# Optimization experiments

Measured on AMD Instinct MI355X. Metric: run time of the kernel, lower is better.

The kernel has to match this reference:

```python
import jax, jax.numpy as jnp
import numpy as np

DIM, NHEADS = 1024, 16
HD = DIM // NHEADS
ROPE_BASE = 10000.0


def rope_cos_sin(seq_len, hd):
    inv_freq = 1.0 / (ROPE_BASE ** (jnp.arange(0, hd, 2, dtype=jnp.float32) / hd))
    t = jnp.arange(seq_len, dtype=jnp.float32)
    freqs = jnp.outer(t, inv_freq)              # [N, hd/2]
    emb = jnp.concatenate([freqs, freqs], -1)   # [N, hd]
    return jnp.cos(emb), jnp.sin(emb)


def rotate_half(x):
    h = x.shape[-1] // 2
    return jnp.concatenate([-x[..., h:], x[..., :h]], -1)


def setup_inputs() -> dict:
    key = jax.random.key(0)
    ks = jax.random.split(key, 5)
    B, N = 1, 2048
    x = jax.random.normal(ks[0], (B, N, DIM), jnp.float32)
    wq = jax.random.normal(ks[1], (DIM, DIM), jnp.float32) * 0.02
    wk = jax.random.normal(ks[2], (DIM, DIM), jnp.float32) * 0.02
    wv = jax.random.normal(ks[3], (DIM, DIM), jnp.float32) * 0.02
    wp = jax.random.normal(ks[4], (DIM, DIM), jnp.float32) * 0.02
    return {"x": x, "wq": wq, "wk": wk, "wv": wv, "wp": wp}


def reference(x, wq, wk, wv, wp):
    B, N, D = x.shape
    H, hd = NHEADS, HD
    # nn.Linear: y = x @ W.T (weights stored [out, in])
    q = (x @ wq.T).reshape(B, N, H, hd)
    k = (x @ wk.T).reshape(B, N, H, hd)
    v = (x @ wv.T).reshape(B, N, H, hd)
    cos, sin = rope_cos_sin(N, hd)
    cos = cos[None, :, None, :]
    sin = sin[None, :, None, :]
    q = q * cos + rotate_half(q) * sin
    k = k * cos + rotate_half(k) * sin
    # SDPA (no mask, non-causal, eval -> no dropout)
    scale = 1.0 / jnp.sqrt(jnp.float32(hd))
    logits = jnp.einsum("bqhd,bkhd->bhqk", q, k) * scale
    attn = jax.nn.softmax(logits, axis=-1)
    out = jnp.einsum("bhqk,bkhd->bqhd", attn, v).reshape(B, N, D)
    return out @ wp.T
```

## Files before the change

### kernel.cpp

```cpp
#include <hip/hip_runtime.h>

typedef short s16x8 __attribute__((ext_vector_type(8)));
typedef float f32x4 __attribute__((ext_vector_type(4)));

__device__ __forceinline__ unsigned short f2bf(float f) {
    unsigned int u = __float_as_uint(f);
    u += 0x7fff + ((u >> 16) & 1);
    return (unsigned short)(u >> 16);
}
__device__ __forceinline__ float bf2f(unsigned short h) {
    return __uint_as_float(((unsigned int)h) << 16);
}
__device__ __forceinline__ f32x4 mfma16(s16x8 a, s16x8 b, f32x4 c) {
    return __builtin_amdgcn_mfma_f32_16x16x32_bf16(a, b, c, 0, 0, 0);
}
__device__ __forceinline__ void async16(const void* g, void* l) {
    __builtin_amdgcn_global_load_lds(
        (const __attribute__((address_space(1))) void*)g,
        (__attribute__((address_space(3))) void*)l, 16, 0, 0);
}

__global__ __launch_bounds__(256) void convert_all(
    const float* __restrict__ x,  const float* __restrict__ wq,
    const float* __restrict__ wk, const float* __restrict__ wv,
    const float* __restrict__ wp,
    unsigned short* __restrict__ xb, unsigned short* __restrict__ wqkvb,
    unsigned short* __restrict__ wpb)
{
    const size_t XN = 2048u * 1024u, WN = 1024u * 1024u;
    size_t e = ((size_t)blockIdx.x * 256 + threadIdx.x) * 4;
    const float* s; unsigned short* d;
    if (e < XN)                { s = x  + e;               d = xb    + e; }
    else if (e < XN + WN)      { s = wq + (e - XN);        d = wqkvb + (e - XN); }
    else if (e < XN + 2 * WN)  { s = wk + (e - XN - WN);   d = wqkvb + (e - XN); }
    else if (e < XN + 3 * WN)  { s = wv + (e - XN - 2*WN); d = wqkvb + (e - XN); }
    else                       { s = wp + (e - XN - 3*WN); d = wpb   + (e - XN - 3*WN); }
    float4 v = *(const float4*)s;
    ushort4 o;
    o.x = f2bf(v.x); o.y = f2bf(v.y); o.z = f2bf(v.z); o.w = f2bf(v.w);
    *(ushort4*)d = o;
}

template<int BM, int BN, int C32>
__global__ __launch_bounds__(256) void gemm_mfma(
    const unsigned short* __restrict__ A,
    const unsigned short* __restrict__ B,
    void* __restrict__ C, int Ntot)
{
    constexpr int MT = BM / 32, NT = BN / 32;
    __shared__ unsigned short As[BM * 64];
    __shared__ unsigned short Bs[BN * 64];

    const int tid  = threadIdx.x;
    const int wave = tid >> 6, lane = tid & 63;
    const int l16  = lane & 15, quad = lane >> 4;
    const int m0   = blockIdx.y * BM, n0 = blockIdx.x * BN;
    const int wm   = (wave & 1) * (BM / 2), wn = (wave >> 1) * (BN / 2);

    const int srow = lane >> 3;
    const int scol = (lane & 7) * 8;

    f32x4 acc[MT][NT] = {};

    for (int k0 = 0; k0 < 1024; k0 += 64) {
        #pragma unroll
        for (int i = 0; i < MT; i++) {
            int j = wave * MT + i;
            async16(A + (size_t)(m0 + j * 8 + srow) * 1024 + k0 + scol, &As[j * 512]);
        }
        #pragma unroll
        for (int i = 0; i < NT; i++) {
            int j = wave * NT + i;
            async16(B + (size_t)(n0 + j * 8 + srow) * 1024 + k0 + scol, &Bs[j * 512]);
        }
        __syncthreads();

        #pragma unroll
        for (int ks = 0; ks < 2; ks++) {
            s16x8 af[MT], bfr[NT];
            #pragma unroll
            for (int mt = 0; mt < MT; mt++)
                af[mt] = *(const s16x8*)&As[(wm + mt * 16 + l16) * 64 + ks * 32 + quad * 8];
            #pragma unroll
            for (int nt = 0; nt < NT; nt++)
                bfr[nt] = *(const s16x8*)&Bs[(wn + nt * 16 + l16) * 64 + ks * 32 + quad * 8];
            #pragma unroll
            for (int mt = 0; mt < MT; mt++)
                #pragma unroll
                for (int nt = 0; nt < NT; nt++)
                    acc[mt][nt] = mfma16(af[mt], bfr[nt], acc[mt][nt]);
        }
        __syncthreads();
    }

    #pragma unroll
    for (int mt = 0; mt < MT; mt++)
        #pragma unroll
        for (int nt = 0; nt < NT; nt++)
            #pragma unroll
            for (int r = 0; r < 4; r++) {
                int m = m0 + wm + mt * 16 + quad * 4 + r;
                int n = n0 + wn + nt * 16 + l16;
                size_t idx = (size_t)m * Ntot + n;
                if (C32) ((float*)C)[idx] = acc[mt][nt][r];
                else     ((unsigned short*)C)[idx] = f2bf(acc[mt][nt][r]);
            }
}

__global__ __launch_bounds__(256) void rope_kernel(unsigned short* __restrict__ qkv)
{
    int idx = blockIdx.x * 256 + threadIdx.x;
    int i = idx & 31;
    int h = (idx >> 5) & 15;
    int n = idx >> 9;
    float ang = (float)n * exp2f((float)i * (-13.287712379549449f / 32.0f));
    float c, s;
    sincosf(ang, &c, &s);
    size_t base = (size_t)n * 3072 + h * 64 + i;
    float a0 = bf2f(qkv[base]), a1 = bf2f(qkv[base + 32]);
    qkv[base]      = f2bf(a0 * c + a1 * s);
    qkv[base + 32] = f2bf(a1 * c - a0 * s);
    float b0 = bf2f(qkv[base + 1024]), b1 = bf2f(qkv[base + 1056]);
    qkv[base + 1024] = f2bf(b0 * c + b1 * s);
    qkv[base + 1056] = f2bf(b1 * c - b0 * s);
}

__global__ __launch_bounds__(256) void attn_part(
    const unsigned short* __restrict__ qkv,
    float* __restrict__ Opart, float* __restrict__ Lpart)
{
    const int h  = blockIdx.y;
    const int q0 = blockIdx.x * 64;
    const int ks = blockIdx.z;
    const int tid  = threadIdx.x;
    const int wave = tid >> 6, lane = tid & 63;
    const int l16  = lane & 15, quad = lane >> 4;

    __shared__ unsigned short Ks[128][72];
    __shared__ unsigned short Vt[64][136];
    __shared__ unsigned short Ps[4][16][136];

    const int mq = q0 + wave * 16 + l16;
    const unsigned short* qp = qkv + (size_t)mq * 3072 + h * 64 + quad * 8;
    s16x8 qa0 = *(const s16x8*)qp;
    s16x8 qa1 = *(const s16x8*)(qp + 32);

    f32x4 o[4] = {};
    float lrow[4] = {0.f, 0.f, 0.f, 0.f};

    const int skey = tid >> 1;
    const int sd   = (tid & 1) * 32;
    const int vg   = tid & 31;
    const int vdo  = (tid >> 5) * 8;

    for (int t8 = 0; t8 < 8; t8++) {
        const int kt = ks * 1024 + t8 * 128;
        {
            const unsigned short* gk = qkv + (size_t)(kt + skey) * 3072 + 1024 + h * 64 + sd;
            const uint4* gk4 = (const uint4*)gk;
            uint4 k0 = gk4[0], k1 = gk4[1], k2 = gk4[2], k3 = gk4[3];
            *(uint4*)&Ks[skey][sd]      = k0;
            *(uint4*)&Ks[skey][sd + 8]  = k1;
            *(uint4*)&Ks[skey][sd + 16] = k2;
            *(uint4*)&Ks[skey][sd + 24] = k3;
        }
        {
            const unsigned short* gv = qkv + (size_t)(kt + 4 * vg) * 3072 + 2048 + h * 64 + vdo;
            unsigned short a0[8], a1[8], a2[8], a3[8];
            *(uint4*)a0 = *(const uint4*)gv;
            *(uint4*)a1 = *(const uint4*)(gv + 3072);
            *(uint4*)a2 = *(const uint4*)(gv + 2 * 3072);
            *(uint4*)a3 = *(const uint4*)(gv + 3 * 3072);
            #pragma unroll
            for (int d = 0; d < 8; d++) {
                ushort4 w;
                w.x = a0[d]; w.y = a1[d]; w.z = a2[d]; w.w = a3[d];
                *(ushort4*)&Vt[vdo + d][4 * vg] = w;
            }
        }
        __syncthreads();

        f32x4 s[8];
        #pragma unroll
        for (int nt = 0; nt < 8; nt++) {
            s16x8 b0 = *(const s16x8*)&Ks[nt * 16 + l16][quad * 8];
            s16x8 b1 = *(const s16x8*)&Ks[nt * 16 + l16][32 + quad * 8];
            f32x4 z = {};
            z = mfma16(qa0, b0, z);
            z = mfma16(qa1, b1, z);
            s[nt] = z;
        }
        #pragma unroll
        for (int nt = 0; nt < 8; nt++)
            #pragma unroll
            for (int r = 0; r < 4; r++) {
                float p = __expf(s[nt][r] * 0.125f);
                lrow[r] += p;
                Ps[wave][quad * 4 + r][nt * 16 + l16] = f2bf(p);
            }

        s16x8 pa[4];
        #pragma unroll
        for (int kc = 0; kc < 4; kc++)
            pa[kc] = *(const s16x8*)&Ps[wave][l16][kc * 32 + quad * 8];

        #pragma unroll
        for (int dt = 0; dt < 4; dt++)
            #pragma unroll
            for (int kc = 0; kc < 4; kc++) {
                s16x8 vb = *(const s16x8*)&Vt[dt * 16 + l16][kc * 32 + quad * 8];
                o[dt] = mfma16(pa[kc], vb, o[dt]);
            }
        __syncthreads();
    }

    #pragma unroll
    for (int r = 0; r < 4; r++) {
        float v = lrow[r];
        #pragma unroll
        for (int off = 8; off >= 1; off >>= 1)
            v += __shfl_xor(v, off, 64);
        lrow[r] = v;
    }
    #pragma unroll
    for (int r = 0; r < 4; r++) {
        int m = q0 + wave * 16 + quad * 4 + r;
        float* op = Opart + ((size_t)ks * 2048 + m) * 1024 + h * 64;
        #pragma unroll
        for (int dt = 0; dt < 4; dt++)
            op[dt * 16 + l16] = o[dt][r];
        if (l16 == 0)
            Lpart[((size_t)ks * 2048 + m) * 16 + h] = lrow[r];
    }
}

__global__ __launch_bounds__(256) void combine(
    const float* __restrict__ Opart, const float* __restrict__ Lpart,
    unsigned short* __restrict__ ab)
{
    size_t e = ((size_t)blockIdx.x * 256 + threadIdx.x) * 4;
    int tok = (int)(e >> 10);
    int h = (int)((e & 1023) >> 6);
    float l = Lpart[(size_t)tok * 16 + h] + Lpart[(size_t)(2048 + tok) * 16 + h];
    float inv = 1.0f / l;
    float4 n0 = *(const float4*)(Opart + e);
    float4 n1 = *(const float4*)(Opart + (size_t)2048 * 1024 + e);
    ushort4 w;
    w.x = f2bf((n0.x + n1.x) * inv);
    w.y = f2bf((n0.y + n1.y) * inv);
    w.z = f2bf((n0.z + n1.z) * inv);
    w.w = f2bf((n0.w + n1.w) * inv);
    *(ushort4*)(ab + e) = w;
}

extern "C" void kernel_launch(void* const* d_in, const int* in_sizes, int n_in,
                              void* d_out, int out_size, void* d_ws, size_t ws_size,
                              hipStream_t stream)
{
    const float* x  = (const float*)d_in[0];
    const float* wq = (const float*)d_in[1];
    const float* wk = (const float*)d_in[2];
    const float* wv = (const float*)d_in[3];
    const float* wp = (const float*)d_in[4];

    unsigned short* xb    = (unsigned short*)d_ws;
    unsigned short* wqkvb = xb    + 2u * 1024 * 1024;
    unsigned short* wpb   = wqkvb + 3u * 1024 * 1024;
    unsigned short* qkv   = wpb   + 1u * 1024 * 1024;
    unsigned short* ab    = qkv   + 2048u * 3072;
    float* Opart = (float*)(ab + 2u * 1024 * 1024);
    float* Lpart = Opart + 2u * 2048 * 1024;

    convert_all<<<6144, 256, 0, stream>>>(x, wq, wk, wv, wp, xb, wqkvb, wpb);
    gemm_mfma<128, 64, 0><<<dim3(48, 16), 256, 0, stream>>>(xb, wqkvb, qkv, 3072);
    rope_kernel<<<(2048 * 512) / 256, 256, 0, stream>>>(qkv);
    attn_part<<<dim3(32, 16, 2), 256, 0, stream>>>(qkv, Opart, Lpart);
    combine<<<2048, 256, 0, stream>>>(Opart, Lpart, ab);
    gemm_mfma<64, 64, 1><<<dim3(16, 32), 256, 0, stream>>>(ab, wpb, d_out, 1024);
}
```

Baseline: 176.6 us.

## Rework attention to 32x32 MFMA with 4-way key split; deepen GEMM K tile

The attention kernel moves from 16x16x32 to 32x32x16 bf16 MFMA. Each wave now handles 32 queries, each block 128 queries, and keys are split four ways into 64-key tiles, with half the threads loading the transposed V and half loading K. The combine kernel now reduces four partial outputs instead of two. The GEMM doubles its K tile to 128, which halves the number of barrier iterations. The aim is better MFMA efficiency and more parallelism in attention, paid for with twice as much partial-output traffic and more LDS per GEMM block.

```diff
diff --git a/kernel.cpp b/kernel.cpp
--- a/kernel.cpp
+++ b/kernel.cpp
@@ -2,6 +2,7 @@
 
 typedef short s16x8 __attribute__((ext_vector_type(8)));
 typedef float f32x4 __attribute__((ext_vector_type(4)));
+typedef float f32x16 __attribute__((ext_vector_type(16)));
 
 __device__ __forceinline__ unsigned short f2bf(float f) {
     unsigned int u = __float_as_uint(f);
@@ -13,6 +14,9 @@
 }
 __device__ __forceinline__ f32x4 mfma16(s16x8 a, s16x8 b, f32x4 c) {
     return __builtin_amdgcn_mfma_f32_16x16x32_bf16(a, b, c, 0, 0, 0);
+}
+__device__ __forceinline__ f32x16 mfma32(s16x8 a, s16x8 b, f32x16 c) {
+    return __builtin_amdgcn_mfma_f32_32x32x16_bf16(a, b, c, 0, 0, 0);
 }
 __device__ __forceinline__ void async16(const void* g, void* l) {
     __builtin_amdgcn_global_load_lds(
@@ -48,8 +52,8 @@
     void* __restrict__ C, int Ntot)
 {
     constexpr int MT = BM / 32, NT = BN / 32;
-    __shared__ unsigned short As[BM * 64];
-    __shared__ unsigned short Bs[BN * 64];
+    __shared__ unsigned short As[BM * 128];
+    __shared__ unsigned short Bs[BN * 128];
 
     const int tid  = threadIdx.x;
     const int wave = tid >> 6, lane = tid & 63;
@@ -57,33 +61,33 @@
     const int m0   = blockIdx.y * BM, n0 = blockIdx.x * BN;
     const int wm   = (wave & 1) * (BM / 2), wn = (wave >> 1) * (BN / 2);
 
-    const int srow = lane >> 3;
-    const int scol = (lane & 7) * 8;
+    const int r4 = lane >> 4;
+    const int c8 = (lane & 15) * 8;
 
     f32x4 acc[MT][NT] = {};
 
-    for (int k0 = 0; k0 < 1024; k0 += 64) {
-        #pragma unroll
-        for (int i = 0; i < MT; i++) {
-            int j = wave * MT + i;
-            async16(A + (size_t)(m0 + j * 8 + srow) * 1024 + k0 + scol, &As[j * 512]);
-        }
-        #pragma unroll
-        for (int i = 0; i < NT; i++) {
-            int j = wave * NT + i;
-            async16(B + (size_t)(n0 + j * 8 + srow) * 1024 + k0 + scol, &Bs[j * 512]);
-        }
-        __syncthreads();
-
-        #pragma unroll
-        for (int ks = 0; ks < 2; ks++) {
+    for (int k0 = 0; k0 < 1024; k0 += 128) {
+        #pragma unroll
+        for (int i = 0; i < BM / 16; i++) {
+            int rg = wave * (BM / 16) + i;
+            async16(A + (size_t)(m0 + rg * 4 + r4) * 1024 + k0 + c8, &As[rg * 512]);
+        }
+        #pragma unroll
+        for (int i = 0; i < BN / 16; i++) {
+            int rg = wave * (BN / 16) + i;
+            async16(B + (size_t)(n0 + rg * 4 + r4) * 1024 + k0 + c8, &Bs[rg * 512]);
+        }
+        __syncthreads();
+
+        #pragma unroll
+        for (int ks = 0; ks < 4; ks++) {
             s16x8 af[MT], bfr[NT];
             #pragma unroll
             for (int mt = 0; mt < MT; mt++)
-                af[mt] = *(const s16x8*)&As[(wm + mt * 16 + l16) * 64 + ks * 32 + quad * 8];
+                af[mt] = *(const s16x8*)&As[(wm + mt * 16 + l16) * 128 + ks * 32 + quad * 8];
             #pragma unroll
             for (int nt = 0; nt < NT; nt++)
-                bfr[nt] = *(const s16x8*)&Bs[(wn + nt * 16 + l16) * 64 + ks * 32 + quad * 8];
+                bfr[nt] = *(const s16x8*)&Bs[(wn + nt * 16 + l16) * 128 + ks * 32 + quad * 8];
             #pragma unroll
             for (int mt = 0; mt < MT; mt++)
                 #pragma unroll
@@ -125,113 +129,107 @@
     qkv[base + 1056] = f2bf(b1 * c - b0 * s);
 }
 
-__global__ __launch_bounds__(256) void attn_part(
+__global__ __launch_bounds__(256, 4) void attn_part(
     const unsigned short* __restrict__ qkv,
     float* __restrict__ Opart, float* __restrict__ Lpart)
 {
     const int h  = blockIdx.y;
-    const int q0 = blockIdx.x * 64;
+    const int q0 = blockIdx.x * 128;
     const int ks = blockIdx.z;
     const int tid  = threadIdx.x;
     const int wave = tid >> 6, lane = tid & 63;
-    const int l16  = lane & 15, quad = lane >> 4;
-
-    __shared__ unsigned short Ks[128][72];
-    __shared__ unsigned short Vt[64][136];
-    __shared__ unsigned short Ps[4][16][136];
-
-    const int mq = q0 + wave * 16 + l16;
-    const unsigned short* qp = qkv + (size_t)mq * 3072 + h * 64 + quad * 8;
-    s16x8 qa0 = *(const s16x8*)qp;
-    s16x8 qa1 = *(const s16x8*)(qp + 32);
-
-    f32x4 o[4] = {};
-    float lrow[4] = {0.f, 0.f, 0.f, 0.f};
-
-    const int skey = tid >> 1;
-    const int sd   = (tid & 1) * 32;
-    const int vg   = tid & 31;
-    const int vdo  = (tid >> 5) * 8;
-
-    for (int t8 = 0; t8 < 8; t8++) {
-        const int kt = ks * 1024 + t8 * 128;
-        {
-            const unsigned short* gk = qkv + (size_t)(kt + skey) * 3072 + 1024 + h * 64 + sd;
-            const uint4* gk4 = (const uint4*)gk;
-            uint4 k0 = gk4[0], k1 = gk4[1], k2 = gk4[2], k3 = gk4[3];
-            *(uint4*)&Ks[skey][sd]      = k0;
-            *(uint4*)&Ks[skey][sd + 8]  = k1;
-            *(uint4*)&Ks[skey][sd + 16] = k2;
-            *(uint4*)&Ks[skey][sd + 24] = k3;
-        }
-        {
-            const unsigned short* gv = qkv + (size_t)(kt + 4 * vg) * 3072 + 2048 + h * 64 + vdo;
+    const int l32  = lane & 31, half = lane >> 5;
+
+    __shared__ unsigned short Ks[64][72];
+    __shared__ unsigned short Vt[64][72];
+    __shared__ unsigned short Ps[4][32][72];
+
+    const unsigned short* qp = qkv + (size_t)(q0 + wave * 32 + l32) * 3072 + h * 64 + half * 8;
+    s16x8 qb[4];
+    #pragma unroll
+    for (int c = 0; c < 4; c++)
+        qb[c] = *(const s16x8*)(qp + c * 16);
+
+    f32x16 o0 = {}, o1 = {};
+    float lsum = 0.f;
+
+    for (int t = 0; t < 8; t++) {
+        const int kt = ks * 512 + t * 64;
+
+        if (tid < 128) {
+            int g  = tid & 15;
+            int d0 = (tid >> 4) * 8;
+            const unsigned short* gv = qkv + (size_t)(kt + 4 * g) * 3072 + 2048 + h * 64 + d0;
             unsigned short a0[8], a1[8], a2[8], a3[8];
             *(uint4*)a0 = *(const uint4*)gv;
             *(uint4*)a1 = *(const uint4*)(gv + 3072);
-            *(uint4*)a2 = *(const uint4*)(gv + 2 * 3072);
-            *(uint4*)a3 = *(const uint4*)(gv + 3 * 3072);
+            *(uint4*)a2 = *(const uint4*)(gv + 6144);
+            *(uint4*)a3 = *(const uint4*)(gv + 9216);
             #pragma unroll
             for (int d = 0; d < 8; d++) {
                 ushort4 w;
                 w.x = a0[d]; w.y = a1[d]; w.z = a2[d]; w.w = a3[d];
-                *(ushort4*)&Vt[vdo + d][4 * vg] = w;
-            }
-        }
-        __syncthreads();
-
-        f32x4 s[8];
-        #pragma unroll
-        for (int nt = 0; nt < 8; nt++) {
-            s16x8 b0 = *(const s16x8*)&Ks[nt * 16 + l16][quad * 8];
-            s16x8 b1 = *(const s16x8*)&Ks[nt * 16 + l16][32 + quad * 8];
-            f32x4 z = {};
-            z = mfma16(qa0, b0, z);
-            z = mfma16(qa1, b1, z);
-            s[nt] = z;
-        }
-        #pragma unroll
-        for (int nt = 0; nt < 8; nt++)
-            #pragma unroll
-            for (int r = 0; r < 4; r++) {
-                float p = __expf(s[nt][r] * 0.125f);
-                lrow[r] += p;
-                Ps[wave][quad * 4 + r][nt * 16 + l16] = f2bf(p);
-            }
-
-        s16x8 pa[4];
-        #pragma unroll
-        for (int kc = 0; kc < 4; kc++)
-            pa[kc] = *(const s16x8*)&Ps[wave][l16][kc * 32 + quad * 8];
-
-        #pragma unroll
-        for (int dt = 0; dt < 4; dt++)
-            #pragma unroll
-            for (int kc = 0; kc < 4; kc++) {
-                s16x8 vb = *(const s16x8*)&Vt[dt * 16 + l16][kc * 32 + quad * 8];
-                o[dt] = mfma16(pa[kc], vb, o[dt]);
-            }
-        __syncthreads();
-    }
-
-    #pragma unroll
-    for (int r = 0; r < 4; r++) {
-        float v = lrow[r];
-        #pragma unroll
-        for (int off = 8; off >= 1; off >>= 1)
-            v += __shfl_xor(v, off, 64);
-        lrow[r] = v;
-    }
-    #pragma unroll
-    for (int r = 0; r < 4; r++) {
-        int m = q0 + wave * 16 + quad * 4 + r;
-        float* op = Opart + ((size_t)ks * 2048 + m) * 1024 + h * 64;
-        #pragma unroll
-        for (int dt = 0; dt < 4; dt++)
-            op[dt * 16 + l16] = o[dt][r];
-        if (l16 == 0)
-            Lpart[((size_t)ks * 2048 + m) * 16 + h] = lrow[r];
-    }
+                *(ushort4*)&Vt[d0 + d][4 * g] = w;
+            }
+        } else {
+            int u = tid - 128;
+            int key = u & 63;
+            int dh = (u >> 6) * 32;
+            const unsigned short* gk = qkv + (size_t)(kt + key) * 3072 + 1024 + h * 64 + dh;
+            const uint4* g4 = (const uint4*)gk;
+            uint4 k0 = g4[0], k1 = g4[1], k2 = g4[2], k3 = g4[3];
+            *(uint4*)&Ks[key][dh]      = k0;
+            *(uint4*)&Ks[key][dh + 8]  = k1;
+            *(uint4*)&Ks[key][dh + 16] = k2;
+            *(uint4*)&Ks[key][dh + 24] = k3;
+        }
+        __syncthreads();
+
+        #pragma unroll
+        for (int g = 0; g < 2; g++) {
+            f32x16 s = {};
+            #pragma unroll
+            for (int c = 0; c < 4; c++) {
+                s16x8 ka = *(const s16x8*)&Ks[g * 32 + l32][c * 16 + half * 8];
+                s = mfma32(ka, qb[c], s);
+            }
+            #pragma unroll
+            for (int c = 0; c < 4; c++) {
+                float e0 = __expf(s[4 * c + 0] * 0.125f);
+                float e1 = __expf(s[4 * c + 1] * 0.125f);
+                float e2 = __expf(s[4 * c + 2] * 0.125f);
+                float e3 = __expf(s[4 * c + 3] * 0.125f);
+                lsum += (e0 + e1) + (e2 + e3);
+                ushort4 w;
+                w.x = f2bf(e0); w.y = f2bf(e1); w.z = f2bf(e2); w.w = f2bf(e3);
+                *(ushort4*)&Ps[wave][l32][g * 32 + c * 8 + half * 4] = w;
+            }
+        }
+
+        #pragma unroll
+        for (int c = 0; c < 4; c++) {
+            s16x8 pa = *(const s16x8*)&Ps[wave][l32][c * 16 + half * 8];
+            s16x8 v0 = *(const s16x8*)&Vt[l32][c * 16 + half * 8];
+            s16x8 v1 = *(const s16x8*)&Vt[32 + l32][c * 16 + half * 8];
+            o0 = mfma32(pa, v0, o0);
+            o1 = mfma32(pa, v1, o1);
+        }
+        __syncthreads();
+    }
+
+    lsum += __shfl_xor(lsum, 32, 64);
+
+    const int mq = q0 + wave * 32;
+    float* opBase = Opart + (size_t)ks * 2048 * 1024;
+    #pragma unroll
+    for (int r = 0; r < 16; r++) {
+        int qr = (r & 3) + 8 * (r >> 2) + 4 * half;
+        float* op = opBase + (size_t)(mq + qr) * 1024 + h * 64;
+        op[l32]      = o0[r];
+        op[32 + l32] = o1[r];
+    }
+    if (half == 0)
+        Lpart[((size_t)ks * 2048 + mq + l32) * 16 + h] = lsum;
 }
 
 __global__ __launch_bounds__(256) void combine(
@@ -241,15 +239,22 @@
     size_t e = ((size_t)blockIdx.x * 256 + threadIdx.x) * 4;
     int tok = (int)(e >> 10);
     int h = (int)((e & 1023) >> 6);
-    float l = Lpart[(size_t)tok * 16 + h] + Lpart[(size_t)(2048 + tok) * 16 + h];
+    float l = 0.f;
+    #pragma unroll
+    for (int s = 0; s < 4; s++)
+        l += Lpart[((size_t)s * 2048 + tok) * 16 + h];
     float inv = 1.0f / l;
-    float4 n0 = *(const float4*)(Opart + e);
-    float4 n1 = *(const float4*)(Opart + (size_t)2048 * 1024 + e);
+    float4 acc = *(const float4*)(Opart + e);
+    #pragma unroll
+    for (int s = 1; s < 4; s++) {
+        float4 n = *(const float4*)(Opart + (size_t)s * 2048 * 1024 + e);
+        acc.x += n.x; acc.y += n.y; acc.z += n.z; acc.w += n.w;
+    }
     ushort4 w;
-    w.x = f2bf((n0.x + n1.x) * inv);
-    w.y = f2bf((n0.y + n1.y) * inv);
-    w.z = f2bf((n0.z + n1.z) * inv);
-    w.w = f2bf((n0.w + n1.w) * inv);
+    w.x = f2bf(acc.x * inv);
+    w.y = f2bf(acc.y * inv);
+    w.z = f2bf(acc.z * inv);
+    w.w = f2bf(acc.w * inv);
     *(ushort4*)(ab + e) = w;
 }
 
@@ -269,12 +274,12 @@
     unsigned short* qkv   = wpb   + 1u * 1024 * 1024;
     unsigned short* ab    = qkv   + 2048u * 3072;
     float* Opart = (float*)(ab + 2u * 1024 * 1024);
-    float* Lpart = Opart + 2u * 2048 * 1024;
+    float* Lpart = Opart + 4u * 2048 * 1024;
 
     convert_all<<<6144, 256, 0, stream>>>(x, wq, wk, wv, wp, xb, wqkvb, wpb);
     gemm_mfma<128, 64, 0><<<dim3(48, 16), 256, 0, stream>>>(xb, wqkvb, qkv, 3072);
     rope_kernel<<<(2048 * 512) / 256, 256, 0, stream>>>(qkv);
-    attn_part<<<dim3(32, 16, 2), 256, 0, stream>>>(qkv, Opart, Lpart);
+    attn_part<<<dim3(16, 16, 4), 256, 0, stream>>>(qkv, Opart, Lpart);
     combine<<<2048, 256, 0, stream>>>(Opart, Lpart, ab);
     gemm_mfma<64, 64, 1><<<dim3(16, 32), 256, 0, stream>>>(ab, wpb, d_out, 1024);
 }
```

Result: no change. 177.5 us (+0.5%).
